# Kernel tuning notes

Measured on AMD Instinct MI355X. Metric: run time of the kernel, lower is better.

Reference implementation:

```python
import jax, jax.numpy as jnp
import numpy as np

B, N, D, NH, MAXLEN = 2, 2048, 1024, 16, 2048
HD = D // NH

def srel_skew(x):
    # x: [B, H, n, n] -> music-transformer skew
    b, h, n, _ = x.shape
    v = jnp.pad(x, ((0, 0), (0, 0), (0, 0), (1, 0)))  # pad last dim left
    return v.reshape(b, h, n + 1, n)[:, :, :n, :]

def split_head(x):
    # [B, n, D] -> [B, H, n, HD]
    b, n, _ = x.shape
    return x.reshape(b, n, NH, HD).transpose(0, 2, 1, 3)

def setup_inputs() -> dict:
    key = jax.random.key(0)
    ks = jax.random.split(key, 7)
    scale = 0.02
    return {
        "x": jax.random.normal(ks[0], (B, N, D), dtype=jnp.float32),
        "Wq": jax.random.normal(ks[1], (D, D), dtype=jnp.float32) * scale,
        "Wk": jax.random.normal(ks[2], (D, D), dtype=jnp.float32) * scale,
        "Wv": jax.random.normal(ks[3], (D, D), dtype=jnp.float32) * scale,
        "Wp": jax.random.normal(ks[4], (D, D), dtype=jnp.float32) * scale,
        "bp": jnp.zeros((D,), dtype=jnp.float32),
        "rel_embed": jax.random.normal(ks[5], (MAXLEN, D), dtype=jnp.float32) * scale,
    }

def reference(x, Wq, Wk, Wv, Wp, bp, rel_embed):
    b, n, d = x.shape
    qx = split_head(x @ Wq.T)  # [B,H,n,HD]
    kx = split_head(x @ Wk.T)
    vx = split_head(x @ Wv.T)
    # relative distance embeddings for last n positions
    ns = jnp.arange(n) + (MAXLEN - n)
    ex = rel_embed[ns].reshape(n, NH, HD).transpose(1, 0, 2)  # [H,n,HD]
    srel = srel_skew(jnp.einsum('bhnd,hmd->bhnm', qx, ex))  # [B,H,n,n]
    inv_dim = 1.0 / np.sqrt(d / NH)
    qk = (jnp.einsum('bhnd,bhmd->bhnm', qx, kx) + srel) * inv_dim
    mask = 1e9 * jnp.triu(jnp.ones((n, n), dtype=x.dtype), 1)
    atten = jax.nn.softmax(qk - mask, axis=-1)
    out = jnp.einsum('bhnm,bhmd->bhnd', atten, vx).transpose(0, 2, 1, 3).reshape(b, n, d)
    return out @ Wp.T + bp
```

## Files before the change

### kernel.cpp

```cpp
#include <hip/hip_runtime.h>

typedef __attribute__((ext_vector_type(8))) short short8;
typedef __attribute__((ext_vector_type(4))) short s16x4;
typedef __attribute__((ext_vector_type(4))) float f32x4;
typedef unsigned short u16t;
typedef unsigned int u32t;

#define MFMA16(a,b,c) __builtin_amdgcn_mfma_f32_16x16x32_bf16((a),(b),(c),0,0,0)

__device__ __forceinline__ f32x4 mfma16x16(s16x4 a, s16x4 b, f32x4 c) {
#if __has_builtin(__builtin_amdgcn_mfma_f32_16x16x16bf16_1k)
  return __builtin_amdgcn_mfma_f32_16x16x16bf16_1k(a, b, c, 0, 0, 0);
#else
  __asm__("v_mfma_f32_16x16x16_bf16 %0, %1, %2, %0" : "+v"(c) : "v"(a), "v"(b));
  return c;
#endif
}

constexpr int Bc = 2, Nc = 2048, Dc = 1024, NHc = 16, HDc = 64;
constexpr int EStride = Nc + 80;

__device__ __forceinline__ u16t f2bf(float f) {
  union { float f; u32t u; } v; v.f = f;
  u32t r = v.u + 0x7FFFu + ((v.u >> 16) & 1u);
  return (u16t)(r >> 16);
}
#if __has_builtin(__builtin_amdgcn_cvt_pk_bf16_f32)
__device__ __forceinline__ u32t pk2(float a, float b) {
  auto r = __builtin_amdgcn_cvt_pk_bf16_f32(a, b);
  return __builtin_bit_cast(u32t, r);
}
#else
__device__ __forceinline__ u32t pk2(float a, float b) {
  u32t ua = __builtin_bit_cast(u32t, a);
  u32t ub = __builtin_bit_cast(u32t, b);
  return ((ua + 0x8000u) >> 16) | ((ub + 0x8000u) & 0xFFFF0000u);
}
#endif
__device__ __forceinline__ s16x4 pk4(float a, float b, float c, float d) {
  union { u32t u[2]; s16x4 s; } r;
  r.u[0] = pk2(a, b); r.u[1] = pk2(c, d);
  return r.s;
}

__device__ __forceinline__ void gld16(const u16t* g, u16t* l) {
  __builtin_amdgcn_global_load_lds(
      (const __attribute__((address_space(1))) unsigned int*)(g),
      (__attribute__((address_space(3))) unsigned int*)(l), 16, 0, 0);
}

__device__ __forceinline__ void cvt4(const float* s, u16t* d) {
  f32x4 v = *(const f32x4*)s;
  u32t* dp = (u32t*)d;
  dp[0] = pk2(v[0], v[1]); dp[1] = pk2(v[2], v[3]);
}

__global__ __launch_bounds__(256) void cvt_all(
    const float* __restrict__ x, const float* __restrict__ wq,
    const float* __restrict__ wk, const float* __restrict__ wv,
    const float* __restrict__ wp, const float* __restrict__ rel,
    u16t* __restrict__ xb, u16t* __restrict__ wqb, u16t* __restrict__ wkb,
    u16t* __restrict__ wvb, u16t* __restrict__ wpb, u16t* __restrict__ Eb) {
  int i = blockIdx.x * 256 + threadIdx.x;
  if (i < 1048576) {
    cvt4(x + (size_t)i * 4, xb + (size_t)i * 4);
  } else if (i < 2097152) {
    int r = i - 1048576;
    int w = r >> 18;
    int k = (r & 262143) * 4;
    const float* s = (w == 0) ? wq : (w == 1) ? wk : (w == 2) ? wv : wp;
    u16t* d = (w == 0) ? wqb : (w == 1) ? wkb : (w == 2) ? wvb : wpb;
    cvt4(s + k, d + k);
  } else if (i < 2621440) {
    int r = i - 2097152;
    int flat = r * 4;
    int h = flat >> 17;
    int rem = flat & 131071;
    int m = rem >> 6, d = rem & 63;
    cvt4(rel + (size_t)m * Dc + h * HDc + d,
         Eb + ((size_t)h * EStride + m) * HDc + d);
  } else {
    int r = i - 2621440;
    int flat = r * 4;
    int h = flat / 5120;
    int rem = flat - h * 5120;
    int pr = rem >> 6, d = rem & 63;
    u32t* dp = (u32t*)(Eb + ((size_t)h * EStride + Nc + pr) * HDc + d);
    dp[0] = 0; dp[1] = 0;
  }
}

__global__ __launch_bounds__(256, 3) void gemm_qkv(const u16t* __restrict__ A,
    const u16t* __restrict__ Wq, const u16t* __restrict__ Wk,
    const u16t* __restrict__ Wv, u16t* __restrict__ Qb,
    u16t* __restrict__ Kb, u16t* __restrict__ Vt) {
  __shared__ u16t lA[128 * 32];
  __shared__ u16t lB[128 * 32];
  const int y = blockIdx.y, which = y >> 3;
  const u16t* W = (which == 0) ? Wq : (which == 1) ? Wk : Wv;
  const float sc = (which == 0) ? 0.18033688011112042f : 1.0f;
  const int m0 = blockIdx.x * 128, n0 = (y & 7) * 128;
  const int t = threadIdx.x, wave = t >> 6, lane = t & 63;
  const int l15 = lane & 15, q4 = lane >> 4, wm = wave & 1, wn = wave >> 1;
  const int srow = wave * 16 + (lane >> 2);
  const int scol = (lane & 3) * 8;

  f32x4 acc[4][4];
  for (int i = 0; i < 4; i++)
    for (int j = 0; j < 4; j++)
      for (int r = 0; r < 4; r++) acc[i][j][r] = 0.f;

  for (int k0 = 0; k0 < Dc; k0 += 32) {
    __syncthreads();
    for (int r = 0; r < 2; r++) {
      int row = srow + r * 64;
      gld16(A + (size_t)(m0 + row) * Dc + k0 + scol, lA + wave * 512 + r * 2048);
      gld16(W + (size_t)(n0 + row) * Dc + k0 + scol, lB + wave * 512 + r * 2048);
    }
    __syncthreads();
    short8 af[4], bf[4];
    for (int i = 0; i < 4; i++) {
      af[i] = *(const short8*)(&lA[(wm * 64 + i * 16 + l15) * 32 + q4 * 8]);
      bf[i] = *(const short8*)(&lB[(wn * 64 + i * 16 + l15) * 32 + q4 * 8]);
    }
    for (int mi = 0; mi < 4; mi++)
      for (int ni = 0; ni < 4; ni++)
        acc[mi][ni] = MFMA16(af[mi], bf[ni], acc[mi][ni]);
  }

  if (which < 2) {
    for (int mi = 0; mi < 4; mi++)
      for (int ni = 0; ni < 4; ni++)
        for (int rg = 0; rg < 4; rg++) {
          int gm = m0 + wm * 64 + mi * 16 + q4 * 4 + rg;
          int gn = n0 + wn * 64 + ni * 16 + l15;
          int b = gm >> 11, n = gm & 2047, h = gn >> 6, hd = gn & 63;
          u16t* outb = (which == 0) ? Qb : Kb;
          outb[(((size_t)(b * NHc + h) * Nc + n) * HDc) + hd] =
              f2bf(acc[mi][ni][rg] * sc);
        }
  } else {
    for (int mi = 0; mi < 4; mi++)
      for (int ni = 0; ni < 4; ni++) {
        int gm = m0 + wm * 64 + mi * 16 + q4 * 4;
        int gn = n0 + wn * 64 + ni * 16 + l15;
        int b = gm >> 11, n = gm & 2047, h = gn >> 6, hd = gn & 63;
        s16x4 pkv = pk4(acc[mi][ni][0], acc[mi][ni][1],
                        acc[mi][ni][2], acc[mi][ni][3]);
        *(s16x4*)(&Vt[((size_t)(b * NHc + h) * HDc + hd) * Nc + n]) = pkv;
      }
  }
}

__global__ __launch_bounds__(256, 2) void gemm_proj(const u16t* __restrict__ A,
    const u16t* __restrict__ W, float* __restrict__ outf,
    const float* __restrict__ bias) {
  __shared__ u16t lA[64 * 32];
  __shared__ u16t lB[128 * 32];
  const int m0 = blockIdx.x * 64, n0 = blockIdx.y * 128;
  const int t = threadIdx.x, wave = t >> 6, lane = t & 63;
  const int l15 = lane & 15, q4 = lane >> 4, wm = wave & 1, wn = wave >> 1;
  const int srow = wave * 16 + (lane >> 2);
  const int scol = (lane & 3) * 8;

  f32x4 acc[2][4];
  for (int i = 0; i < 2; i++)
    for (int j = 0; j < 4; j++)
      for (int r = 0; r < 4; r++) acc[i][j][r] = 0.f;

  for (int k0 = 0; k0 < Dc; k0 += 32) {
    __syncthreads();
    gld16(A + (size_t)(m0 + srow) * Dc + k0 + scol, lA + wave * 512);
    for (int r = 0; r < 2; r++) {
      int row = srow + r * 64;
      gld16(W + (size_t)(n0 + row) * Dc + k0 + scol, lB + wave * 512 + r * 2048);
    }
    __syncthreads();
    short8 af[2], bf[4];
    for (int i = 0; i < 2; i++)
      af[i] = *(const short8*)(&lA[(wm * 32 + i * 16 + l15) * 32 + q4 * 8]);
    for (int i = 0; i < 4; i++)
      bf[i] = *(const short8*)(&lB[(wn * 64 + i * 16 + l15) * 32 + q4 * 8]);
    for (int mi = 0; mi < 2; mi++)
      for (int ni = 0; ni < 4; ni++)
        acc[mi][ni] = MFMA16(af[mi], bf[ni], acc[mi][ni]);
  }

  for (int mi = 0; mi < 2; mi++)
    for (int ni = 0; ni < 4; ni++)
      for (int rg = 0; rg < 4; rg++) {
        int gm = m0 + wm * 32 + mi * 16 + q4 * 4 + rg;
        int gn = n0 + wn * 64 + ni * 16 + l15;
        outf[(size_t)gm * Dc + gn] = acc[mi][ni][rg] + bias[gn];
      }
}

__global__ __launch_bounds__(256, 2) void attn(const u16t* __restrict__ Qb,
                                               const u16t* __restrict__ Kb,
                                               const u16t* __restrict__ Vt,
                                               const u16t* __restrict__ Eb,
                                               u16t* __restrict__ AO) {
  __shared__ u16t lK[64 * 72];
  __shared__ u16t lE[128 * 72];
  __shared__ u16t lV[64 * 72];
  __shared__ float Ps[4][16 * 84];

  const int xbk = blockIdx.x;
  const int h = blockIdx.y, b = blockIdx.z;
  const u16t* Qh = Qb + (size_t)(b * NHc + h) * Nc * HDc;
  const u16t* Kh = Kb + (size_t)(b * NHc + h) * Nc * HDc;
  const u16t* Vh = Vt + (size_t)(b * NHc + h) * HDc * Nc;
  const u16t* Eh = Eb + (size_t)h * EStride * HDc;

  const int t = threadIdx.x, wave = t >> 6, lane = t & 63, l15 = lane & 15, q4 = lane >> 4;
  const int tbase = (3 - wave) * 16;
  const int Tm = wave * 16 + l15;
  float* Pw = Ps[wave];

  const int sr = t >> 3, sc8 = (t & 7) * 8;
  const int sr2 = sr + 32;

  for (int ph = 0; ph < 2; ph++) {
    const int qi = ph ? xbk : (31 - xbk);
    const int r0 = qi * 64;
    const int rw = r0 + wave * 16;

    short8 qf[2], qsf[2];
    {
      int r = rw + l15;
      int rs = r - 1; if (rs < 0) rs = 0;
      for (int kh = 0; kh < 2; kh++) {
        qf[kh]  = *(const short8*)(Qh + (size_t)r * HDc + kh * 32 + q4 * 8);
        qsf[kh] = *(const short8*)(Qh + (size_t)rs * HDc + kh * 32 + q4 * 8);
      }
    }

    f32x4 accO[4];
    float l_p = 0.f;
    for (int dt = 0; dt < 4; dt++)
      for (int rg = 0; rg < 4; rg++) accO[dt][rg] = 0.f;

    auto body = [&](int j, bool last) {
      f32x4 accS[4];
      for (int ct = 0; ct < 4; ct++)
        for (int rg = 0; rg < 4; rg++) accS[ct][rg] = 0.f;
      for (int kh = 0; kh < 2; kh++)
        for (int ct = 0; ct < 4; ct++) {
          short8 kfr = *(const short8*)(&lK[(ct * 16 + l15) * 72 + kh * 32 + q4 * 8]);
          accS[ct] = MFMA16(kfr, qf[kh], accS[ct]);
        }
      const int rot = (j & 1) << 6;
      f32x4 accP[5];
      for (int pt = 0; pt < 5; pt++)
        for (int rg = 0; rg < 4; rg++) accP[pt][rg] = 0.f;
      for (int kh = 0; kh < 2; kh++)
        for (int pt = 0; pt < 5; pt++) {
          int prow = (tbase + pt * 16 + l15 + rot) & 127;
          short8 efr = *(const short8*)(&lE[prow * 72 + kh * 32 + q4 * 8]);
          accP[pt] = MFMA16(efr, qsf[kh], accP[pt]);
        }
      for (int pt = 0; pt < 5; pt++)
        *(f32x4*)(&Pw[l15 * 84 + pt * 16 + q4 * 4]) = accP[pt];
      __asm__ volatile("s_waitcnt lgkmcnt(0)" ::: "memory");
      const int rbase = l15 * 83 + q4 * 4 + 15;
      float pv[4][4];
      for (int ct = 0; ct < 4; ct++)
        for (int rg = 0; rg < 4; rg++) {
          float s = accS[ct][rg] + Pw[rbase + ct * 16 + rg];
          if (last && (ct * 16 + q4 * 4 + rg) > Tm) s = -1e30f;
          float p = exp2f(s);
          l_p += p;
          pv[ct][rg] = p;
        }
      __asm__ volatile("" ::: "memory");
      s16x4 bq[4];
      for (int ks = 0; ks < 4; ks++)
        bq[ks] = pk4(pv[ks][0], pv[ks][1], pv[ks][2], pv[ks][3]);
      for (int dt = 0; dt < 4; dt++)
        for (int ks = 0; ks < 4; ks++) {
          s16x4 vfr = *(const s16x4*)(&lV[(dt * 16 + l15) * 72 + ks * 16 + q4 * 4]);
          accO[dt] = mfma16x16(vfr, bq[ks], accO[dt]);
        }
    };

    {
      *(f32x4*)(&lK[sr * 72 + sc8])  = *(const f32x4*)(Kh + (size_t)sr * HDc + sc8);
      *(f32x4*)(&lK[sr2 * 72 + sc8]) = *(const f32x4*)(Kh + (size_t)sr2 * HDc + sc8);
      *(f32x4*)(&lV[sr * 72 + sc8])  = *(const f32x4*)(Vh + (size_t)sr * Nc + sc8);
      *(f32x4*)(&lV[sr2 * 72 + sc8]) = *(const f32x4*)(Vh + (size_t)sr2 * Nc + sc8);
      const int ebase0 = Nc - 63 - r0;
      for (int i = 0; i < 4; i++) {
        int cc = t + i * 256;
        int s = cc >> 3, c8 = (cc & 7) * 8;
        *(f32x4*)(&lE[s * 72 + c8]) =
            *(const f32x4*)(Eh + (size_t)(ebase0 + s) * HDc + c8);
      }
    }

    for (int j = 0; j < qi; j++) {
      __syncthreads();
      const int cn = j * 64 + 64;
      f32x4 pK0 = *(const f32x4*)(Kh + (size_t)(cn + sr) * HDc + sc8);
      f32x4 pK1 = *(const f32x4*)(Kh + (size_t)(cn + sr2) * HDc + sc8);
      f32x4 pV0 = *(const f32x4*)(Vh + (size_t)sr * Nc + cn + sc8);
      f32x4 pV1 = *(const f32x4*)(Vh + (size_t)sr2 * Nc + cn + sc8);
      const int ebn = 64 * (j + 1) - r0 + (Nc - 63) + 64;
      f32x4 pE0 = *(const f32x4*)(Eh + (size_t)(ebn + sr) * HDc + sc8);
      f32x4 pE1 = *(const f32x4*)(Eh + (size_t)(ebn + sr2) * HDc + sc8);

      body(j, false);

      __syncthreads();
      *(f32x4*)(&lK[sr * 72 + sc8])  = pK0;
      *(f32x4*)(&lK[sr2 * 72 + sc8]) = pK1;
      *(f32x4*)(&lV[sr * 72 + sc8])  = pV0;
      *(f32x4*)(&lV[sr2 * 72 + sc8]) = pV1;
      int ph0 = (sr + 64 * j) & 127;
      int ph1 = (sr2 + 64 * j) & 127;
      *(f32x4*)(&lE[ph0 * 72 + sc8]) = pE0;
      *(f32x4*)(&lE[ph1 * 72 + sc8]) = pE1;
    }

    __syncthreads();
    body(qi, true);

    float l2 = l_p + __shfl_xor(l_p, 16);
    float lt = l2 + __shfl_xor(l2, 32);
    float inv = 1.f / lt;
    {
      int r = rw + l15;
      u16t* dst = AO + (size_t)(b * Nc + r) * Dc + h * HDc + q4 * 4;
      for (int dt = 0; dt < 4; dt++) {
        s16x4 o = pk4(accO[dt][0] * inv, accO[dt][1] * inv,
                      accO[dt][2] * inv, accO[dt][3] * inv);
        *(s16x4*)(dst + dt * 16) = o;
      }
    }
  }
}

extern "C" void kernel_launch(void* const* d_in, const int* in_sizes, int n_in,
                              void* d_out, int out_size, void* d_ws, size_t ws_size,
                              hipStream_t stream) {
  (void)in_sizes; (void)n_in; (void)out_size; (void)ws_size;
  const float* x   = (const float*)d_in[0];
  const float* Wq  = (const float*)d_in[1];
  const float* Wk  = (const float*)d_in[2];
  const float* Wv  = (const float*)d_in[3];
  const float* Wp  = (const float*)d_in[4];
  const float* bp  = (const float*)d_in[5];
  const float* rel = (const float*)d_in[6];
  float* out = (float*)d_out;

  char* ws = (char*)d_ws;
  u16t* xb  = (u16t*)(ws);
  u16t* wqb = (u16t*)(ws + 8388608);
  u16t* wkb = (u16t*)(ws + 10485760);
  u16t* wvb = (u16t*)(ws + 12582912);
  u16t* wpb = (u16t*)(ws + 14680064);
  u16t* Eb  = (u16t*)(ws + 16777216);
  u16t* Qb  = (u16t*)(ws + 21233664);
  u16t* Kb  = (u16t*)(ws + 29622272);
  u16t* Vtb = (u16t*)(ws + 38010880);
  u16t* AOb = (u16t*)(ws + 46399488);

  cvt_all<<<10320, 256, 0, stream>>>(x, Wq, Wk, Wv, Wp, rel,
                                     xb, wqb, wkb, wvb, wpb, Eb);
  gemm_qkv<<<dim3(32, 24), 256, 0, stream>>>(xb, wqb, wkb, wvb, Qb, Kb, Vtb);
  attn<<<dim3(16, NHc, Bc), 256, 0, stream>>>(Qb, Kb, Vtb, Eb, AOb);
  gemm_proj<<<dim3(64, 8), 256, 0, stream>>>(AOb, wpb, out, bp);
}
```

Measured before the change: 212.9 us.

## Double-buffer K/V in LDS and load E fragments directly from global

```diff
diff --git a/kernel.cpp b/kernel.cpp
--- a/kernel.cpp
+++ b/kernel.cpp
@@ -200,9 +200,8 @@
                                                const u16t* __restrict__ Vt,
                                                const u16t* __restrict__ Eb,
                                                u16t* __restrict__ AO) {
-  __shared__ u16t lK[64 * 72];
-  __shared__ u16t lE[128 * 72];
-  __shared__ u16t lV[64 * 72];
+  __shared__ u16t lK[2][64 * 72];
+  __shared__ u16t lV[2][64 * 72];
   __shared__ float Ps[4][16 * 84];
 
   const int xbk = blockIdx.x;
@@ -219,6 +218,7 @@
 
   const int sr = t >> 3, sc8 = (t & 7) * 8;
   const int sr2 = sr + 32;
+  const u16t* Ew = Eh + (size_t)(tbase + l15) * HDc + q4 * 8;
 
   for (int ph = 0; ph < 2; ph++) {
     const int qi = ph ? xbk : (31 - xbk);
@@ -240,25 +240,28 @@
     for (int dt = 0; dt < 4; dt++)
       for (int rg = 0; rg < 4; rg++) accO[dt][rg] = 0.f;
 
-    auto body = [&](int j, bool last) {
+    auto body = [&](int j, int buf, bool last) {
+      const u16t* lKb = lK[buf];
+      const u16t* lVb = lV[buf];
+      const int eb = 64 * j - r0 + (Nc - 63);
+      short8 efr[2][5];
+      for (int kh = 0; kh < 2; kh++)
+        for (int pt = 0; pt < 5; pt++)
+          efr[kh][pt] = *(const short8*)(Ew + ((size_t)(eb + pt * 16)) * HDc + kh * 32);
       f32x4 accS[4];
       for (int ct = 0; ct < 4; ct++)
         for (int rg = 0; rg < 4; rg++) accS[ct][rg] = 0.f;
       for (int kh = 0; kh < 2; kh++)
         for (int ct = 0; ct < 4; ct++) {
-          short8 kfr = *(const short8*)(&lK[(ct * 16 + l15) * 72 + kh * 32 + q4 * 8]);
+          short8 kfr = *(const short8*)(&lKb[(ct * 16 + l15) * 72 + kh * 32 + q4 * 8]);
           accS[ct] = MFMA16(kfr, qf[kh], accS[ct]);
         }
-      const int rot = (j & 1) << 6;
       f32x4 accP[5];
       for (int pt = 0; pt < 5; pt++)
         for (int rg = 0; rg < 4; rg++) accP[pt][rg] = 0.f;
       for (int kh = 0; kh < 2; kh++)
-        for (int pt = 0; pt < 5; pt++) {
-          int prow = (tbase + pt * 16 + l15 + rot) & 127;
-          short8 efr = *(const short8*)(&lE[prow * 72 + kh * 32 + q4 * 8]);
-          accP[pt] = MFMA16(efr, qsf[kh], accP[pt]);
-        }
+        for (int pt = 0; pt < 5; pt++)
+          accP[pt] = MFMA16(efr[kh][pt], qsf[kh], accP[pt]);
       for (int pt = 0; pt < 5; pt++)
         *(f32x4*)(&Pw[l15 * 84 + pt * 16 + q4 * 4]) = accP[pt];
       __asm__ volatile("s_waitcnt lgkmcnt(0)" ::: "memory");
@@ -278,23 +281,17 @@
         bq[ks] = pk4(pv[ks][0], pv[ks][1], pv[ks][2], pv[ks][3]);
       for (int dt = 0; dt < 4; dt++)
         for (int ks = 0; ks < 4; ks++) {
-          s16x4 vfr = *(const s16x4*)(&lV[(dt * 16 + l15) * 72 + ks * 16 + q4 * 4]);
+          s16x4 vfr = *(const s16x4*)(&lVb[(dt * 16 + l15) * 72 + ks * 16 + q4 * 4]);
           accO[dt] = mfma16x16(vfr, bq[ks], accO[dt]);
         }
     };
 
+    __syncthreads();
     {
-      *(f32x4*)(&lK[sr * 72 + sc8])  = *(const f32x4*)(Kh + (size_t)sr * HDc + sc8);
-      *(f32x4*)(&lK[sr2 * 72 + sc8]) = *(const f32x4*)(Kh + (size_t)sr2 * HDc + sc8);
-      *(f32x4*)(&lV[sr * 72 + sc8])  = *(const f32x4*)(Vh + (size_t)sr * Nc + sc8);
-      *(f32x4*)(&lV[sr2 * 72 + sc8]) = *(const f32x4*)(Vh + (size_t)sr2 * Nc + sc8);
-      const int ebase0 = Nc - 63 - r0;
-      for (int i = 0; i < 4; i++) {
-        int cc = t + i * 256;
-        int s = cc >> 3, c8 = (cc & 7) * 8;
-        *(f32x4*)(&lE[s * 72 + c8]) =
-            *(const f32x4*)(Eh + (size_t)(ebase0 + s) * HDc + c8);
-      }
+      *(f32x4*)(&lK[0][sr * 72 + sc8])  = *(const f32x4*)(Kh + (size_t)sr * HDc + sc8);
+      *(f32x4*)(&lK[0][sr2 * 72 + sc8]) = *(const f32x4*)(Kh + (size_t)sr2 * HDc + sc8);
+      *(f32x4*)(&lV[0][sr * 72 + sc8])  = *(const f32x4*)(Vh + (size_t)sr * Nc + sc8);
+      *(f32x4*)(&lV[0][sr2 * 72 + sc8]) = *(const f32x4*)(Vh + (size_t)sr2 * Nc + sc8);
     }
 
     for (int j = 0; j < qi; j++) {
@@ -304,25 +301,18 @@
       f32x4 pK1 = *(const f32x4*)(Kh + (size_t)(cn + sr2) * HDc + sc8);
       f32x4 pV0 = *(const f32x4*)(Vh + (size_t)sr * Nc + cn + sc8);
       f32x4 pV1 = *(const f32x4*)(Vh + (size_t)sr2 * Nc + cn + sc8);
-      const int ebn = 64 * (j + 1) - r0 + (Nc - 63) + 64;
-      f32x4 pE0 = *(const f32x4*)(Eh + (size_t)(ebn + sr) * HDc + sc8);
-      f32x4 pE1 = *(const f32x4*)(Eh + (size_t)(ebn + sr2) * HDc + sc8);
-
-      body(j, false);
-
-      __syncthreads();
-      *(f32x4*)(&lK[sr * 72 + sc8])  = pK0;
-      *(f32x4*)(&lK[sr2 * 72 + sc8]) = pK1;
-      *(f32x4*)(&lV[sr * 72 + sc8])  = pV0;
-      *(f32x4*)(&lV[sr2 * 72 + sc8]) = pV1;
-      int ph0 = (sr + 64 * j) & 127;
-      int ph1 = (sr2 + 64 * j) & 127;
-      *(f32x4*)(&lE[ph0 * 72 + sc8]) = pE0;
-      *(f32x4*)(&lE[ph1 * 72 + sc8]) = pE1;
-    }
-
-    __syncthreads();
-    body(qi, true);
+
+      body(j, j & 1, false);
+
+      const int nb = (j + 1) & 1;
+      *(f32x4*)(&lK[nb][sr * 72 + sc8])  = pK0;
+      *(f32x4*)(&lK[nb][sr2 * 72 + sc8]) = pK1;
+      *(f32x4*)(&lV[nb][sr * 72 + sc8])  = pV0;
+      *(f32x4*)(&lV[nb][sr2 * 72 + sc8]) = pV1;
+    }
+
+    __syncthreads();
+    body(qi, qi & 1, true);
 
     float l2 = l_p + __shfl_xor(l_p, 16);
     float lt = l2 + __shfl_xor(l2, 32);
```

Result: slower. 246.9 us (+15.9%).
